# Performance work log

Hardware: AMD Instinct MI355X
Metric: run time of the kernel (lower is better)

Reference implementation:

```python
import jax, jax.numpy as jnp
import numpy as np

B, V, C, CD, D, H, W = 1, 3, 32, 8, 32, 128, 160
LAMB = 1.5


def _bilinear(img, x, y):
    # img: [c, Hs, Ws]; x, y: pixel coords [D, HW]; zero padding, align_corners=True semantics
    c, Hs, Ws = img.shape
    x0 = jnp.floor(x)
    y0 = jnp.floor(y)
    x0i = x0.astype(jnp.int32)
    y0i = y0.astype(jnp.int32)
    wx = x - x0
    wy = y - y0
    imgf = img.reshape(c, Hs * Ws)

    def gather(xi, yi, w):
        valid = (xi >= 0) & (xi < Ws) & (yi >= 0) & (yi < Hs)
        lin = jnp.clip(yi, 0, Hs - 1) * Ws + jnp.clip(xi, 0, Ws - 1)
        v = jnp.take(imgf, lin.reshape(-1), axis=1).reshape((c,) + xi.shape)
        return v * (w * valid.astype(w.dtype))[None]

    return (gather(x0i, y0i, (1 - wx) * (1 - wy))
            + gather(x0i + 1, y0i, wx * (1 - wy))
            + gather(x0i, y0i + 1, (1 - wx) * wy)
            + gather(x0i + 1, y0i + 1, wx * wy))


def _homo_warp(src_fea, src_proj, ref_proj, depth_values):
    # src_fea [B,c,Hs,Ws]; projs [B,4,4]; depth_values [B,D,H,W] -> [B,c,D,H,W]
    b, c, Hs, Ws = src_fea.shape
    _, d, h, w = depth_values.shape
    proj = jnp.einsum('bij,bjk->bik', src_proj, jnp.linalg.inv(ref_proj))
    rot = proj[:, :3, :3]
    tr = proj[:, :3, 3]
    ys, xs = jnp.meshgrid(jnp.arange(h, dtype=src_fea.dtype), jnp.arange(w, dtype=src_fea.dtype), indexing='ij')
    xyz = jnp.stack([xs.reshape(-1), ys.reshape(-1), jnp.ones(h * w, dtype=src_fea.dtype)], 0)  # [3,HW]
    rx = jnp.einsum('bij,jn->bin', rot, xyz)  # [B,3,HW]
    dvals = depth_values.reshape(b, 1, d, h * w)
    pxyz = rx[:, :, None, :] * dvals + tr[:, :, None, None]  # [B,3,D,HW]
    z = pxyz[:, 2]
    px = pxyz[:, 0] / z  # [B,D,HW]
    py = pxyz[:, 1] / z
    out = jax.vmap(_bilinear)(src_fea, px, py)  # [B,c,D,HW]
    return out.reshape(b, c, d, h, w)


def setup_inputs() -> dict:
    key = jax.random.key(0)
    k1, k2, k3 = jax.random.split(key, 3)
    features = jax.random.normal(k1, (V, B, C, H, W), jnp.float32)
    deps_feature_stage = jax.random.normal(k2, (V, B, CD, H, W), jnp.float32)
    reg_w = jax.random.normal(k3, (1, C + CD), jnp.float32) * 0.1
    K = np.array([[200., 0., W / 2.], [0., 200., H / 2.], [0., 0., 1.]])
    mats = []
    for tx in [0.0, 1.0, -1.0]:
        Rt = np.eye(4)
        Rt[0, 3] = tx
        P = np.eye(4)
        P[:3, :4] = K @ Rt[:3, :4]
        mats.append(P)
    proj_matrices = jnp.asarray(np.stack(mats)[None], jnp.float32)  # [B,V,4,4]
    depth_values = jnp.broadcast_to(
        jnp.linspace(5.0, 10.0, D, dtype=jnp.float32)[None, :, None, None], (B, D, H, W)) + jnp.zeros((B, D, H, W), jnp.float32)
    return {'features': features, 'deps_feature_stage': deps_feature_stage,
            'proj_matrices': proj_matrices, 'depth_values': depth_values,
            'reg_w': reg_w, 'num_depth': D, 'stage_idx': 0}


def reference(features, deps_feature_stage, proj_matrices, depth_values, reg_w, num_depth, stage_idx):
    num_views = features.shape[0]
    d = depth_values.shape[1]
    ref_proj = proj_matrices[:, 0]

    def variance_volume(feats):
        ref = feats[0]  # [B,c,H,W]
        ref_vol = jnp.broadcast_to(ref[:, :, None], (ref.shape[0], ref.shape[1], d, ref.shape[2], ref.shape[3]))
        s = ref_vol
        sq = ref_vol * ref_vol
        for v in range(1, num_views):
            wv = _homo_warp(feats[v], proj_matrices[:, v], ref_proj, depth_values)
            s = s + wv
            sq = sq + wv * wv
        return sq / num_views - (s / num_views) ** 2

    volume_variance = variance_volume(features)      # [B,C,D,H,W]
    deps_variance = variance_volume(deps_feature_stage)  # [B,CD,D,H,W]
    var = jnp.concatenate([volume_variance, deps_variance], axis=1)
    # cost_regularization modeled as 1x1x1 conv reducing channels to 1
    cost = jnp.einsum('bcdhw,oc->bodhw', var, reg_w)[:, 0]  # [B,D,H,W]
    prob_volume = jax.nn.softmax(cost, axis=1)
    depth = jnp.sum(prob_volume * depth_values, axis=1)  # [B,H,W]
    samp_variance = (depth_values - depth[:, None]) ** 2
    exp_variance = LAMB * jnp.sqrt(jnp.sum(samp_variance * prob_volume, axis=1))
    return depth, exp_variance, prob_volume
```

## Files before the change

kernel.cpp:

```cpp
#include <hip/hip_runtime.h>
#include <math.h>

#define HH   128
#define WW   160
#define HWN  (HH*WW)
#define NCF  32
#define NCD  8
#define ND   32
#define NV   3
#define LAMBF 1.5f

template <int CH>
__device__ void transpose_tile(const float* __restrict__ src, float* __restrict__ dst,
                               float (*lds)[33], int tid) {
    for (int i = tid; i < CH*8; i += 256) {
        int c = i >> 3, xg = (i & 7) << 2;
        *(float4*)&lds[c][xg] = *(const float4*)(src + c*HWN + xg);
    }
    __syncthreads();
    for (int i = tid; i < 32*(CH/4); i += 256) {
        int xl = i / (CH/4), c4 = (i % (CH/4)) * 4;
        float4 t = make_float4(lds[c4][xl], lds[c4+1][xl], lds[c4+2][xl], lds[c4+3][xl]);
        *(float4*)(dst + xl*CH + c4) = t;
    }
}

__global__ __launch_bounds__(256) void prep_k(const float* __restrict__ feat,
                                              const float* __restrict__ deps,
                                              const float* __restrict__ proj,
                                              float* __restrict__ featT,
                                              float* __restrict__ depsT,
                                              float* __restrict__ projw) {
    if (blockIdx.x == 0 && blockIdx.y == 0 && blockIdx.z == 0 && threadIdx.x == 0) {
        float M00 = proj[0], M01 = proj[1], M02 = proj[2],  m0 = proj[3];
        float M10 = proj[4], M11 = proj[5], M12 = proj[6],  m1 = proj[7];
        float M20 = proj[8], M21 = proj[9], M22 = proj[10], m2 = proj[11];
        float c00 =  (M11*M22 - M12*M21);
        float c01 = -(M10*M22 - M12*M20);
        float c02 =  (M10*M21 - M11*M20);
        float det = M00*c00 + M01*c01 + M02*c02;
        float id  = 1.f / det;
        float i00 = c00*id, i01 = -(M01*M22 - M02*M21)*id, i02 =  (M01*M12 - M02*M11)*id;
        float i10 = c01*id, i11 =  (M00*M22 - M02*M20)*id, i12 = -(M00*M12 - M02*M10)*id;
        float i20 = c02*id, i21 = -(M00*M21 - M01*M20)*id, i22 =  (M00*M11 - M01*M10)*id;
        float t0 = -(i00*m0 + i01*m1 + i02*m2);
        float t1 = -(i10*m0 + i11*m1 + i12*m2);
        float t2 = -(i20*m0 + i21*m1 + i22*m2);
        #pragma unroll
        for (int v = 1; v < NV; v++) {
            const float* S = proj + v*16;
            float s00 = S[0], s01 = S[1], s02 = S[2],  st0 = S[3];
            float s10 = S[4], s11 = S[5], s12 = S[6],  st1 = S[7];
            float s20 = S[8], s21 = S[9], s22 = S[10], st2 = S[11];
            float* o = projw + (v-1)*12;
            o[0] = s00*i00 + s01*i10 + s02*i20;
            o[1] = s00*i01 + s01*i11 + s02*i21;
            o[2] = s00*i02 + s01*i12 + s02*i22;
            o[3] = s10*i00 + s11*i10 + s12*i20;
            o[4] = s10*i01 + s11*i11 + s12*i21;
            o[5] = s10*i02 + s11*i12 + s12*i22;
            o[6] = s20*i00 + s21*i10 + s22*i20;
            o[7] = s20*i01 + s21*i11 + s22*i21;
            o[8] = s20*i02 + s21*i12 + s22*i22;
            o[9]  = s00*t0 + s01*t1 + s02*t2 + st0;
            o[10] = s10*t0 + s11*t1 + s12*t2 + st1;
            o[11] = s20*t0 + s21*t1 + s22*t2 + st2;
        }
    }

    __shared__ float lds[NCF][33];
    const int z  = blockIdx.z;
    const int xb = blockIdx.x * 32;
    const int y  = blockIdx.y;
    if (z < NV) {
        transpose_tile<NCF>(feat + (size_t)(z*NCF)*HWN + y*WW + xb,
                            featT + (size_t)(z*HWN + y*WW + xb) * NCF,
                            lds, threadIdx.x);
    } else {
        transpose_tile<NCD>(deps + (size_t)((z - NV)*NCD)*HWN + y*WW + xb,
                            depsT + (size_t)((z - NV)*HWN + y*WW + xb) * NCD,
                            lds, threadIdx.x);
    }
}

__global__ __launch_bounds__(256) void cost_volume_k(
    const float* __restrict__ featT,
    const float* __restrict__ depsT,
    const float* __restrict__ dvals,
    const float* __restrict__ regw,
    const float* __restrict__ pws,
    float* __restrict__ out)
{
    __shared__ float cl [ND][9];
    __shared__ float dvl[ND][9];
    __shared__ float smax[8], sisum[8];

    const int t    = threadIdx.x;
    const int lane = t & 63;
    const int wid  = t >> 6;
    const int cg   = lane & 7;
    const int pl   = lane >> 3;
    const int pixg = blockIdx.x * 8 + pl;
    const int y    = pixg / WW;
    const int x    = pixg - y * WW;
    const float fx = (float)x, fy = (float)y;
    const int dbase = wid * 8;

    float RX[2], RY[2], RZ[2], T0[2], T1[2], T2[2];
    #pragma unroll
    for (int v = 0; v < 2; v++) {
        const float* q = pws + v*12;
        RX[v] = q[0]*fx + q[1]*fy + q[2];
        RY[v] = q[3]*fx + q[4]*fy + q[5];
        RZ[v] = q[6]*fx + q[7]*fy + q[8];
        T0[v] = q[9]; T1[v] = q[10]; T2[v] = q[11];
    }

    auto bsetup = [&](float dvv, int v, int CH, float& w00, float& w10,
                      float& w01, float& w11, int& o00, int& o10,
                      int& o01, int& o11) {
        float pz = RZ[v]*dvv + T2[v];
        float iz = __builtin_amdgcn_rcpf(pz);
        float px = (RX[v]*dvv + T0[v]) * iz;
        float py = (RY[v]*dvv + T1[v]) * iz;
        float x0f = floorf(px), y0f = floorf(py);
        int x0 = (int)x0f, y0 = (int)y0f;
        float wx = px - x0f, wy = py - y0f;
        float omx = 1.f - wx, omy = 1.f - wy;
        bool vx0 = (x0 >= 0) & (x0 < WW);
        bool vx1 = (x0+1 >= 0) & (x0+1 < WW);
        bool vy0 = (y0 >= 0) & (y0 < HH);
        bool vy1 = (y0+1 >= 0) & (y0+1 < HH);
        w00 = (vx0 && vy0) ? omx*omy : 0.f;
        w10 = (vx1 && vy0) ? wx*omy  : 0.f;
        w01 = (vx0 && vy1) ? omx*wy  : 0.f;
        w11 = (vx1 && vy1) ? wx*wy   : 0.f;
        int xc0 = min(max(x0,   0), WW-1);
        int xc1 = min(max(x0+1, 0), WW-1);
        int yc0 = min(max(y0,   0), HH-1);
        int yc1 = min(max(y0+1, 0), HH-1);
        o00 = (yc0*WW + xc0)*CH;
        o10 = (yc0*WW + xc1)*CH;
        o01 = (yc1*WW + xc0)*CH;
        o11 = (yc1*WW + xc1)*CH;
    };

    {
        float dvv_own = dvals[(dbase + cg)*HWN + pixg];
        dvl[dbase + cg][pl] = dvv_own;
        float SW00[2], SW10[2], SW01[2], SW11[2];
        int   SO00[2], SO10[2], SO01[2], SO11[2];
        #pragma unroll
        for (int v = 0; v < 2; v++)
            bsetup(dvv_own, v, NCF, SW00[v], SW10[v], SW01[v], SW11[v],
                   SO00[v], SO10[v], SO01[v], SO11[v]);

        float4 r4 = *(const float4*)(featT + (size_t)pixg*NCF + cg*4);
        float4 w4 = *(const float4*)(regw + cg*4);
        const float wca0 = w4.x*(1.f/3.f), wca1 = w4.y*(1.f/3.f),
                    wca2 = w4.z*(1.f/3.f), wca3 = w4.w*(1.f/3.f);
        const float wcb0 = w4.x*(1.f/9.f), wcb1 = w4.y*(1.f/9.f),
                    wcb2 = w4.z*(1.f/9.f), wcb3 = w4.w*(1.f/9.f);
        const float rx0 = r4.x, rx1 = r4.y, rx2 = r4.z, rx3 = r4.w;
        const float* b1 = featT + (size_t)1*HWN*NCF + cg*4;
        const float* b2 = featT + (size_t)2*HWN*NCF + cg*4;
        const int plbase = lane & 0x38;

        #pragma unroll 2
        for (int jj = 0; jj < 8; jj++) {
            const int src = plbase | jj;
            float s0 = rx0, s1 = rx1, s2 = rx2, s3 = rx3;
            float q0 = rx0*rx0, q1 = rx1*rx1, q2 = rx2*rx2, q3 = rx3*rx3;

            #pragma unroll
            for (int v = 0; v < 2; v++) {
                float W00 = __shfl(SW00[v], src, 64);
                float W10 = __shfl(SW10[v], src, 64);
                float W01 = __shfl(SW01[v], src, 64);
                float W11 = __shfl(SW11[v], src, 64);
                int   o00 = __shfl(SO00[v], src, 64);
                int   o10 = __shfl(SO10[v], src, 64);
                int   o01 = __shfl(SO01[v], src, 64);
                int   o11 = __shfl(SO11[v], src, 64);
                const float* b = v ? b2 : b1;
                float4 f00 = *(const float4*)(b + o00);
                float4 f10 = *(const float4*)(b + o10);
                float4 f01 = *(const float4*)(b + o01);
                float4 f11 = *(const float4*)(b + o11);
                float wv0 = W00*f00.x + W10*f10.x + W01*f01.x + W11*f11.x;
                float wv1 = W00*f00.y + W10*f10.y + W01*f01.y + W11*f11.y;
                float wv2 = W00*f00.z + W10*f10.z + W01*f01.z + W11*f11.z;
                float wv3 = W00*f00.w + W10*f10.w + W01*f01.w + W11*f11.w;
                s0 += wv0; q0 = fmaf(wv0, wv0, q0);
                s1 += wv1; q1 = fmaf(wv1, wv1, q1);
                s2 += wv2; q2 = fmaf(wv2, wv2, q2);
                s3 += wv3; q3 = fmaf(wv3, wv3, q3);
            }
            float part = wca0*q0 - wcb0*s0*s0;
            part = fmaf(wca1, q1, part); part = fmaf(-wcb1, s1*s1, part);
            part = fmaf(wca2, q2, part); part = fmaf(-wcb2, s2*s2, part);
            part = fmaf(wca3, q3, part); part = fmaf(-wcb3, s3*s3, part);
            part += __shfl_xor(part, 1);
            part += __shfl_xor(part, 2);
            part += __shfl_xor(part, 4);
            if (cg == jj) cl[dbase + jj][pl] = part;
        }
    }
    __syncthreads();

    {
        const int cgd  = lane & 1;
        const int dsub = (lane >> 1) & 3;
        float4 r4 = *(const float4*)(depsT + (size_t)pixg*NCD + cgd*4);
        float4 w4 = *(const float4*)(regw + NCF + cgd*4);
        const float wca0 = w4.x*(1.f/3.f), wca1 = w4.y*(1.f/3.f),
                    wca2 = w4.z*(1.f/3.f), wca3 = w4.w*(1.f/3.f);
        const float wcb0 = w4.x*(1.f/9.f), wcb1 = w4.y*(1.f/9.f),
                    wcb2 = w4.z*(1.f/9.f), wcb3 = w4.w*(1.f/9.f);
        const float rx0 = r4.x, rx1 = r4.y, rx2 = r4.z, rx3 = r4.w;
        const float* b1 = depsT + (size_t)1*HWN*NCD + cgd*4;
        const float* b2 = depsT + (size_t)2*HWN*NCD + cgd*4;

        #pragma unroll
        for (int i = 0; i < 2; i++) {
            const int d = dbase + dsub + 4*i;
            float dvv = dvl[d][pl];
            float s0 = rx0, s1 = rx1, s2 = rx2, s3 = rx3;
            float q0 = rx0*rx0, q1 = rx1*rx1, q2 = rx2*rx2, q3 = rx3*rx3;

            #pragma unroll
            for (int v = 0; v < 2; v++) {
                float W00, W10, W01, W11; int o00, o10, o01, o11;
                bsetup(dvv, v, NCD, W00, W10, W01, W11, o00, o10, o01, o11);
                const float* b = v ? b2 : b1;
                float4 f00 = *(const float4*)(b + o00);
                float4 f10 = *(const float4*)(b + o10);
                float4 f01 = *(const float4*)(b + o01);
                float4 f11 = *(const float4*)(b + o11);
                float wv0 = W00*f00.x + W10*f10.x + W01*f01.x + W11*f11.x;
                float wv1 = W00*f00.y + W10*f10.y + W01*f01.y + W11*f11.y;
                float wv2 = W00*f00.z + W10*f10.z + W01*f01.z + W11*f11.z;
                float wv3 = W00*f00.w + W10*f10.w + W01*f01.w + W11*f11.w;
                s0 += wv0; q0 = fmaf(wv0, wv0, q0);
                s1 += wv1; q1 = fmaf(wv1, wv1, q1);
                s2 += wv2; q2 = fmaf(wv2, wv2, q2);
                s3 += wv3; q3 = fmaf(wv3, wv3, q3);
            }
            float part = wca0*q0 - wcb0*s0*s0;
            part = fmaf(wca1, q1, part); part = fmaf(-wcb1, s1*s1, part);
            part = fmaf(wca2, q2, part); part = fmaf(-wcb2, s2*s2, part);
            part = fmaf(wca3, q3, part); part = fmaf(-wcb3, s3*s3, part);
            part += __shfl_xor(part, 1);
            if (cgd == 0) cl[d][pl] += part;
        }
    }
    __syncthreads();

    if (t < 8) {
        const int plx  = t;
        const int pixo = blockIdx.x * 8 + plx;
        float m = -1e30f;
        #pragma unroll
        for (int d = 0; d < ND; d++) m = fmaxf(m, cl[d][plx]);
        float sum = 0.f, pd = 0.f, pd2 = 0.f;
        #pragma unroll
        for (int d = 0; d < ND; d++) {
            float e   = __expf(cl[d][plx] - m);
            float dvv = dvl[d][plx];
            sum += e;
            pd  = fmaf(e, dvv, pd);
            pd2 = fmaf(e, dvv*dvv, pd2);
        }
        float isum  = 1.f / sum;
        float depth = pd * isum;
        float sv    = pd2 * isum - depth*depth;
        float ev    = LAMBF * sqrtf(fmaxf(sv, 0.f));
        smax[plx]  = m;
        sisum[plx] = isum;
        out[pixo]       = depth;
        out[HWN + pixo] = ev;
    }
    __syncthreads();
    {
        const int plx  = t & 7;
        const int dd   = t >> 3;
        const int pixo = blockIdx.x * 8 + plx;
        out[2*HWN + dd*HWN + pixo] = __expf(cl[dd][plx] - smax[plx]) * sisum[plx];
    }
}

extern "C" void kernel_launch(void* const* d_in, const int* in_sizes, int n_in,
                              void* d_out, int out_size, void* d_ws, size_t ws_size,
                              hipStream_t stream) {
    const float* features = (const float*)d_in[0];
    const float* deps     = (const float*)d_in[1];
    const float* proj     = (const float*)d_in[2];
    const float* dvals    = (const float*)d_in[3];
    const float* regw     = (const float*)d_in[4];

    float* ws    = (float*)d_ws;
    float* projw = ws;
    float* featT = ws + 64;
    float* depsT = featT + (size_t)NV*HWN*NCF;

    dim3 tg(WW/32, HH, 2*NV);
    prep_k<<<tg, 256, 0, stream>>>(features, deps, proj, featT, depsT, projw);

    cost_volume_k<<<HWN/8, 256, 0, stream>>>(featT, depsT, dvals, regw, projw,
                                             (float*)d_out);
}
```

Baseline: 103.9 us.

## Store transposed features in fp16 and reuse bilinear setup for depth features

The transposed feature copies are now stored as half precision, which halves the bytes written by the prep kernel and read by the gather in the cost-volume kernel. Bilinear interpolation is done with packed half2 FMAs before widening to float for the variance accumulation. The depth-feature pass no longer recomputes the projection setup; it shuffles the precomputed offsets and weights from the main pass and shifts the offsets to its smaller channel stride. A __syncthreads before that pass is dropped. Half-precision weights and features reduce accuracy, which may matter for the softmax output tolerance.

```diff
diff --git a/kernel.cpp b/kernel.cpp
--- a/kernel.cpp
+++ b/kernel.cpp
@@ -1,4 +1,5 @@
 #include <hip/hip_runtime.h>
+#include <hip/hip_fp16.h>
 #include <math.h>
 
 #define HH   128
@@ -11,7 +12,7 @@
 #define LAMBF 1.5f
 
 template <int CH>
-__device__ void transpose_tile(const float* __restrict__ src, float* __restrict__ dst,
+__device__ void transpose_tile(const float* __restrict__ src, __half* __restrict__ dst,
                                float (*lds)[33], int tid) {
     for (int i = tid; i < CH*8; i += 256) {
         int c = i >> 3, xg = (i & 7) << 2;
@@ -20,16 +21,18 @@
     __syncthreads();
     for (int i = tid; i < 32*(CH/4); i += 256) {
         int xl = i / (CH/4), c4 = (i % (CH/4)) * 4;
-        float4 t = make_float4(lds[c4][xl], lds[c4+1][xl], lds[c4+2][xl], lds[c4+3][xl]);
-        *(float4*)(dst + xl*CH + c4) = t;
+        __half2 h0 = __floats2half2_rn(lds[c4][xl],   lds[c4+1][xl]);
+        __half2 h1 = __floats2half2_rn(lds[c4+2][xl], lds[c4+3][xl]);
+        uint2 u; u.x = *(unsigned*)&h0; u.y = *(unsigned*)&h1;
+        *(uint2*)(dst + xl*CH + c4) = u;
     }
 }
 
 __global__ __launch_bounds__(256) void prep_k(const float* __restrict__ feat,
                                               const float* __restrict__ deps,
                                               const float* __restrict__ proj,
-                                              float* __restrict__ featT,
-                                              float* __restrict__ depsT,
+                                              __half* __restrict__ featH,
+                                              __half* __restrict__ depsH,
                                               float* __restrict__ projw) {
     if (blockIdx.x == 0 && blockIdx.y == 0 && blockIdx.z == 0 && threadIdx.x == 0) {
         float M00 = proj[0], M01 = proj[1], M02 = proj[2],  m0 = proj[3];
@@ -74,18 +77,18 @@
     const int y  = blockIdx.y;
     if (z < NV) {
         transpose_tile<NCF>(feat + (size_t)(z*NCF)*HWN + y*WW + xb,
-                            featT + (size_t)(z*HWN + y*WW + xb) * NCF,
+                            featH + (size_t)(z*HWN + y*WW + xb) * NCF,
                             lds, threadIdx.x);
     } else {
         transpose_tile<NCD>(deps + (size_t)((z - NV)*NCD)*HWN + y*WW + xb,
-                            depsT + (size_t)((z - NV)*HWN + y*WW + xb) * NCD,
+                            depsH + (size_t)((z - NV)*HWN + y*WW + xb) * NCD,
                             lds, threadIdx.x);
     }
 }
 
 __global__ __launch_bounds__(256) void cost_volume_k(
-    const float* __restrict__ featT,
-    const float* __restrict__ depsT,
+    const __half* __restrict__ featH,
+    const __half* __restrict__ depsH,
     const float* __restrict__ dvals,
     const float* __restrict__ regw,
     const float* __restrict__ pws,
@@ -105,6 +108,7 @@
     const int x    = pixg - y * WW;
     const float fx = (float)x, fy = (float)y;
     const int dbase = wid * 8;
+    const int plbase = lane & 0x38;
 
     float RX[2], RY[2], RZ[2], T0[2], T1[2], T2[2];
     #pragma unroll
@@ -116,55 +120,79 @@
         T0[v] = q[9]; T1[v] = q[10]; T2[v] = q[11];
     }
 
-    auto bsetup = [&](float dvv, int v, int CH, float& w00, float& w10,
-                      float& w01, float& w11, int& o00, int& o10,
-                      int& o01, int& o11) {
-        float pz = RZ[v]*dvv + T2[v];
-        float iz = __builtin_amdgcn_rcpf(pz);
-        float px = (RX[v]*dvv + T0[v]) * iz;
-        float py = (RY[v]*dvv + T1[v]) * iz;
-        float x0f = floorf(px), y0f = floorf(py);
-        int x0 = (int)x0f, y0 = (int)y0f;
-        float wx = px - x0f, wy = py - y0f;
-        float omx = 1.f - wx, omy = 1.f - wy;
-        bool vx0 = (x0 >= 0) & (x0 < WW);
-        bool vx1 = (x0+1 >= 0) & (x0+1 < WW);
-        bool vy0 = (y0 >= 0) & (y0 < HH);
-        bool vy1 = (y0+1 >= 0) & (y0+1 < HH);
-        w00 = (vx0 && vy0) ? omx*omy : 0.f;
-        w10 = (vx1 && vy0) ? wx*omy  : 0.f;
-        w01 = (vx0 && vy1) ? omx*wy  : 0.f;
-        w11 = (vx1 && vy1) ? wx*wy   : 0.f;
-        int xc0 = min(max(x0,   0), WW-1);
-        int xc1 = min(max(x0+1, 0), WW-1);
-        int yc0 = min(max(y0,   0), HH-1);
-        int yc1 = min(max(y0+1, 0), HH-1);
-        o00 = (yc0*WW + xc0)*CH;
-        o10 = (yc0*WW + xc1)*CH;
-        o01 = (yc1*WW + xc0)*CH;
-        o11 = (yc1*WW + xc1)*CH;
-    };
-
+    int SW00[2], SW10[2], SW01[2], SW11[2];
+    int SO00[2], SO10[2], SO01[2], SO11[2];
     {
         float dvv_own = dvals[(dbase + cg)*HWN + pixg];
         dvl[dbase + cg][pl] = dvv_own;
-        float SW00[2], SW10[2], SW01[2], SW11[2];
-        int   SO00[2], SO10[2], SO01[2], SO11[2];
-        #pragma unroll
-        for (int v = 0; v < 2; v++)
-            bsetup(dvv_own, v, NCF, SW00[v], SW10[v], SW01[v], SW11[v],
-                   SO00[v], SO10[v], SO01[v], SO11[v]);
-
-        float4 r4 = *(const float4*)(featT + (size_t)pixg*NCF + cg*4);
-        float4 w4 = *(const float4*)(regw + cg*4);
+        #pragma unroll
+        for (int v = 0; v < 2; v++) {
+            float pz = RZ[v]*dvv_own + T2[v];
+            float iz = __builtin_amdgcn_rcpf(pz);
+            float px = (RX[v]*dvv_own + T0[v]) * iz;
+            float py = (RY[v]*dvv_own + T1[v]) * iz;
+            float x0f = floorf(px), y0f = floorf(py);
+            int x0 = (int)x0f, y0 = (int)y0f;
+            float wx = px - x0f, wy = py - y0f;
+            float omx = 1.f - wx, omy = 1.f - wy;
+            bool vx0 = (x0 >= 0) & (x0 < WW);
+            bool vx1 = (x0+1 >= 0) & (x0+1 < WW);
+            bool vy0 = (y0 >= 0) & (y0 < HH);
+            bool vy1 = (y0+1 >= 0) & (y0+1 < HH);
+            float W00 = (vx0 && vy0) ? omx*omy : 0.f;
+            float W10 = (vx1 && vy0) ? wx*omy  : 0.f;
+            float W01 = (vx0 && vy1) ? omx*wy  : 0.f;
+            float W11 = (vx1 && vy1) ? wx*wy   : 0.f;
+            __half2 h;
+            h = __float2half2_rn(W00); SW00[v] = *(int*)&h;
+            h = __float2half2_rn(W10); SW10[v] = *(int*)&h;
+            h = __float2half2_rn(W01); SW01[v] = *(int*)&h;
+            h = __float2half2_rn(W11); SW11[v] = *(int*)&h;
+            int xc0 = min(max(x0,   0), WW-1);
+            int xc1 = min(max(x0+1, 0), WW-1);
+            int yc0 = min(max(y0,   0), HH-1);
+            int yc1 = min(max(y0+1, 0), HH-1);
+            SO00[v] = (yc0*WW + xc0)*NCF;
+            SO10[v] = (yc0*WW + xc1)*NCF;
+            SO01[v] = (yc1*WW + xc0)*NCF;
+            SO11[v] = (yc1*WW + xc1)*NCF;
+        }
+    }
+
+    #define INTERP(BPTR, O00, O10, O01, O11, W00p, W10p, W01p, W11p)          \
+        {                                                                      \
+            uint2 u00 = *(const uint2*)(BPTR + O00);                           \
+            uint2 u10 = *(const uint2*)(BPTR + O10);                           \
+            uint2 u01 = *(const uint2*)(BPTR + O01);                           \
+            uint2 u11 = *(const uint2*)(BPTR + O11);                           \
+            __half2 wva = __hmul2(*(__half2*)&u00.x, W00p);                    \
+            wva = __hfma2(*(__half2*)&u10.x, W10p, wva);                       \
+            wva = __hfma2(*(__half2*)&u01.x, W01p, wva);                       \
+            wva = __hfma2(*(__half2*)&u11.x, W11p, wva);                       \
+            __half2 wvb = __hmul2(*(__half2*)&u00.y, W00p);                    \
+            wvb = __hfma2(*(__half2*)&u10.y, W10p, wvb);                       \
+            wvb = __hfma2(*(__half2*)&u01.y, W01p, wvb);                       \
+            wvb = __hfma2(*(__half2*)&u11.y, W11p, wvb);                       \
+            float2 fa = __half22float2(wva);                                   \
+            float2 fb = __half22float2(wvb);                                   \
+            s0 += fa.x; q0 = fmaf(fa.x, fa.x, q0);                             \
+            s1 += fa.y; q1 = fmaf(fa.y, fa.y, q1);                             \
+            s2 += fb.x; q2 = fmaf(fb.x, fb.x, q2);                             \
+            s3 += fb.y; q3 = fmaf(fb.y, fb.y, q3);                             \
+        }
+
+    {
+        uint2 ur = *(const uint2*)(featH + (size_t)pixg*NCF + cg*4);
+        float2 ra = __half22float2(*(__half2*)&ur.x);
+        float2 rb = __half22float2(*(__half2*)&ur.y);
+        const float rx0 = ra.x, rx1 = ra.y, rx2 = rb.x, rx3 = rb.y;
+        const float4 w4 = *(const float4*)(regw + cg*4);
         const float wca0 = w4.x*(1.f/3.f), wca1 = w4.y*(1.f/3.f),
                     wca2 = w4.z*(1.f/3.f), wca3 = w4.w*(1.f/3.f);
         const float wcb0 = w4.x*(1.f/9.f), wcb1 = w4.y*(1.f/9.f),
                     wcb2 = w4.z*(1.f/9.f), wcb3 = w4.w*(1.f/9.f);
-        const float rx0 = r4.x, rx1 = r4.y, rx2 = r4.z, rx3 = r4.w;
-        const float* b1 = featT + (size_t)1*HWN*NCF + cg*4;
-        const float* b2 = featT + (size_t)2*HWN*NCF + cg*4;
-        const int plbase = lane & 0x38;
+        const __half* b1 = featH + (size_t)1*HWN*NCF + cg*4;
+        const __half* b2 = featH + (size_t)2*HWN*NCF + cg*4;
 
         #pragma unroll 2
         for (int jj = 0; jj < 8; jj++) {
@@ -174,27 +202,18 @@
 
             #pragma unroll
             for (int v = 0; v < 2; v++) {
-                float W00 = __shfl(SW00[v], src, 64);
-                float W10 = __shfl(SW10[v], src, 64);
-                float W01 = __shfl(SW01[v], src, 64);
-                float W11 = __shfl(SW11[v], src, 64);
-                int   o00 = __shfl(SO00[v], src, 64);
-                int   o10 = __shfl(SO10[v], src, 64);
-                int   o01 = __shfl(SO01[v], src, 64);
-                int   o11 = __shfl(SO11[v], src, 64);
-                const float* b = v ? b2 : b1;
-                float4 f00 = *(const float4*)(b + o00);
-                float4 f10 = *(const float4*)(b + o10);
-                float4 f01 = *(const float4*)(b + o01);
-                float4 f11 = *(const float4*)(b + o11);
-                float wv0 = W00*f00.x + W10*f10.x + W01*f01.x + W11*f11.x;
-                float wv1 = W00*f00.y + W10*f10.y + W01*f01.y + W11*f11.y;
-                float wv2 = W00*f00.z + W10*f10.z + W01*f01.z + W11*f11.z;
-                float wv3 = W00*f00.w + W10*f10.w + W01*f01.w + W11*f11.w;
-                s0 += wv0; q0 = fmaf(wv0, wv0, q0);
-                s1 += wv1; q1 = fmaf(wv1, wv1, q1);
-                s2 += wv2; q2 = fmaf(wv2, wv2, q2);
-                s3 += wv3; q3 = fmaf(wv3, wv3, q3);
+                int w00i = __shfl(SW00[v], src, 64);
+                int w10i = __shfl(SW10[v], src, 64);
+                int w01i = __shfl(SW01[v], src, 64);
+                int w11i = __shfl(SW11[v], src, 64);
+                int o00  = __shfl(SO00[v], src, 64);
+                int o10  = __shfl(SO10[v], src, 64);
+                int o01  = __shfl(SO01[v], src, 64);
+                int o11  = __shfl(SO11[v], src, 64);
+                __half2 W00p = *(__half2*)&w00i, W10p = *(__half2*)&w10i;
+                __half2 W01p = *(__half2*)&w01i, W11p = *(__half2*)&w11i;
+                const __half* b = v ? b2 : b1;
+                INTERP(b, o00, o10, o01, o11, W00p, W10p, W01p, W11p)
             }
             float part = wca0*q0 - wcb0*s0*s0;
             part = fmaf(wca1, q1, part); part = fmaf(-wcb1, s1*s1, part);
@@ -206,45 +225,44 @@
             if (cg == jj) cl[dbase + jj][pl] = part;
         }
     }
-    __syncthreads();
 
     {
         const int cgd  = lane & 1;
         const int dsub = (lane >> 1) & 3;
-        float4 r4 = *(const float4*)(depsT + (size_t)pixg*NCD + cgd*4);
-        float4 w4 = *(const float4*)(regw + NCF + cgd*4);
+        uint2 ur = *(const uint2*)(depsH + (size_t)pixg*NCD + cgd*4);
+        float2 ra = __half22float2(*(__half2*)&ur.x);
+        float2 rb = __half22float2(*(__half2*)&ur.y);
+        const float rx0 = ra.x, rx1 = ra.y, rx2 = rb.x, rx3 = rb.y;
+        const float4 w4 = *(const float4*)(regw + NCF + cgd*4);
         const float wca0 = w4.x*(1.f/3.f), wca1 = w4.y*(1.f/3.f),
                     wca2 = w4.z*(1.f/3.f), wca3 = w4.w*(1.f/3.f);
         const float wcb0 = w4.x*(1.f/9.f), wcb1 = w4.y*(1.f/9.f),
                     wcb2 = w4.z*(1.f/9.f), wcb3 = w4.w*(1.f/9.f);
-        const float rx0 = r4.x, rx1 = r4.y, rx2 = r4.z, rx3 = r4.w;
-        const float* b1 = depsT + (size_t)1*HWN*NCD + cgd*4;
-        const float* b2 = depsT + (size_t)2*HWN*NCD + cgd*4;
+        const __half* b1 = depsH + (size_t)1*HWN*NCD + cgd*4;
+        const __half* b2 = depsH + (size_t)2*HWN*NCD + cgd*4;
 
         #pragma unroll
         for (int i = 0; i < 2; i++) {
-            const int d = dbase + dsub + 4*i;
-            float dvv = dvl[d][pl];
+            const int jj = dsub + 4*i;
+            const int d  = dbase + jj;
+            const int src = plbase | jj;
             float s0 = rx0, s1 = rx1, s2 = rx2, s3 = rx3;
             float q0 = rx0*rx0, q1 = rx1*rx1, q2 = rx2*rx2, q3 = rx3*rx3;
 
             #pragma unroll
             for (int v = 0; v < 2; v++) {
-                float W00, W10, W01, W11; int o00, o10, o01, o11;
-                bsetup(dvv, v, NCD, W00, W10, W01, W11, o00, o10, o01, o11);
-                const float* b = v ? b2 : b1;
-                float4 f00 = *(const float4*)(b + o00);
-                float4 f10 = *(const float4*)(b + o10);
-                float4 f01 = *(const float4*)(b + o01);
-                float4 f11 = *(const float4*)(b + o11);
-                float wv0 = W00*f00.x + W10*f10.x + W01*f01.x + W11*f11.x;
-                float wv1 = W00*f00.y + W10*f10.y + W01*f01.y + W11*f11.y;
-                float wv2 = W00*f00.z + W10*f10.z + W01*f01.z + W11*f11.z;
-                float wv3 = W00*f00.w + W10*f10.w + W01*f01.w + W11*f11.w;
-                s0 += wv0; q0 = fmaf(wv0, wv0, q0);
-                s1 += wv1; q1 = fmaf(wv1, wv1, q1);
-                s2 += wv2; q2 = fmaf(wv2, wv2, q2);
-                s3 += wv3; q3 = fmaf(wv3, wv3, q3);
+                int w00i = __shfl(SW00[v], src, 64);
+                int w10i = __shfl(SW10[v], src, 64);
+                int w01i = __shfl(SW01[v], src, 64);
+                int w11i = __shfl(SW11[v], src, 64);
+                int o00  = __shfl(SO00[v], src, 64) >> 2;
+                int o10  = __shfl(SO10[v], src, 64) >> 2;
+                int o01  = __shfl(SO01[v], src, 64) >> 2;
+                int o11  = __shfl(SO11[v], src, 64) >> 2;
+                __half2 W00p = *(__half2*)&w00i, W10p = *(__half2*)&w10i;
+                __half2 W01p = *(__half2*)&w01i, W11p = *(__half2*)&w11i;
+                const __half* b = v ? b2 : b1;
+                INTERP(b, o00, o10, o01, o11, W00p, W10p, W01p, W11p)
             }
             float part = wca0*q0 - wcb0*s0*s0;
             part = fmaf(wca1, q1, part); part = fmaf(-wcb1, s1*s1, part);
@@ -298,14 +316,14 @@
     const float* dvals    = (const float*)d_in[3];
     const float* regw     = (const float*)d_in[4];
 
-    float* ws    = (float*)d_ws;
-    float* projw = ws;
-    float* featT = ws + 64;
-    float* depsT = featT + (size_t)NV*HWN*NCF;
+    float*  ws    = (float*)d_ws;
+    float*  projw = ws;
+    __half* featH = (__half*)(ws + 64);
+    __half* depsH = featH + (size_t)NV*HWN*NCF;
 
     dim3 tg(WW/32, HH, 2*NV);
-    prep_k<<<tg, 256, 0, stream>>>(features, deps, proj, featT, depsT, projw);
-
-    cost_volume_k<<<HWN/8, 256, 0, stream>>>(featT, depsT, dvals, regw, projw,
+    prep_k<<<tg, 256, 0, stream>>>(features, deps, proj, featH, depsH, projw);
+
+    cost_volume_k<<<HWN/8, 256, 0, stream>>>(featH, depsH, dvals, regw, projw,
                                              (float*)d_out);
 }
```

Result: no change. 103.0 us (-0.8%).
